# Performance work log

Measured on AMD Instinct MI355X. Metric: run time of the kernel, lower is better.

Reference implementation:

```python
import jax, jax.numpy as jnp
import numpy as np

H = 256       # hidden_dim
DICT = 30     # dict_size
SOS = 1       # symb2int['<sos>']

def gru_cell(x, h, Wih, Whh, bih, bhh):
    # PyTorch GRU cell math
    gi = x @ Wih.T + bih
    gh = h @ Whh.T + bhh
    ir, iz, inn = jnp.split(gi, 3, axis=-1)
    hr, hz, hn = jnp.split(gh, 3, axis=-1)
    r = jax.nn.sigmoid(ir + hr)
    z = jax.nn.sigmoid(iz + hz)
    n = jnp.tanh(inn + r * hn)
    return (1.0 - z) * n + z * h

def run_gru(xs, h0, Wih, Whh, bih, bhh):
    # xs: [T, B, F] -> outputs [T, B, Hc], final hidden [B, Hc]
    def step(h, x):
        h = gru_cell(x, h, Wih, Whh, bih, bhh)
        return h, h
    hT, out = jax.lax.scan(step, h0, xs)
    return out, hT

def setup_inputs() -> dict:
    key = jax.random.key(0)
    ks = jax.random.split(key, 24)
    B, T, L = 128, 512, 64
    se = 1.0 / np.sqrt(H)        # encoder GRU init scale
    sd = 1.0 / np.sqrt(2 * H)    # decoder GRU / linears scale
    def r(k, shape, sc):
        return jax.random.normal(k, shape, jnp.float32) * sc
    return {
        "x": jax.random.normal(ks[0], (B, T, 2), jnp.float32),
        "target_seq": jax.random.randint(ks[1], (B, L), 0, DICT),
        # encoder GRU, forward direction
        "enc_Wih_f": r(ks[2], (3 * H, 2), se), "enc_Whh_f": r(ks[3], (3 * H, H), se),
        "enc_bih_f": r(ks[4], (3 * H,), se),   "enc_bhh_f": r(ks[5], (3 * H,), se),
        # encoder GRU, backward direction
        "enc_Wih_b": r(ks[6], (3 * H, 2), se), "enc_Whh_b": r(ks[7], (3 * H, H), se),
        "enc_bih_b": r(ks[8], (3 * H,), se),   "enc_bhh_b": r(ks[9], (3 * H,), se),
        # decoder embedding + GRU (hidden 2H)
        "emb": r(ks[10], (DICT, H), 1.0),
        "dec_Wih": r(ks[11], (6 * H, H), sd),     "dec_Whh": r(ks[12], (6 * H, 2 * H), sd),
        "dec_bih": r(ks[13], (6 * H,), sd),       "dec_bhh": r(ks[14], (6 * H,), sd),
        # hidden2query, att_combine, fc
        "Wq": r(ks[15], (2 * H, 2 * H), sd), "bq": r(ks[16], (2 * H,), sd),
        "Wc": r(ks[17], (H, 4 * H), sd),     "bc": r(ks[18], (H,), sd),
        "Wf": r(ks[19], (DICT, H), se),      "bf": r(ks[20], (DICT,), se),
    }

def reference(x, target_seq,
              enc_Wih_f, enc_Whh_f, enc_bih_f, enc_bhh_f,
              enc_Wih_b, enc_Whh_b, enc_bih_b, enc_bhh_b,
              emb, dec_Wih, dec_Whh, dec_bih, dec_bhh,
              Wq, bq, Wc, bc, Wf, bf):
    B = x.shape[0]
    xs = jnp.transpose(x, (1, 0, 2))                # [T, B, 2]
    h0 = jnp.zeros((B, H), x.dtype)
    out_f, hf = run_gru(xs, h0, enc_Wih_f, enc_Whh_f, enc_bih_f, enc_bhh_f)
    out_b, hb = run_gru(xs[::-1], h0, enc_Wih_b, enc_Whh_b, enc_bih_b, enc_bhh_b)
    enc_out = jnp.concatenate([out_f, out_b[::-1]], axis=-1)  # [T, B, 2H]
    enc_out = jnp.transpose(enc_out, (1, 0, 2))               # [B, T, 2H]
    hidden = jnp.concatenate([hf, hb], axis=-1)               # [B, 2H]

    # teacher-forced decoder inputs: <sos>, target[0], ..., target[L-2]
    sos = jnp.full((B, 1), SOS, target_seq.dtype)
    toks = jnp.concatenate([sos, target_seq[:, :-1]], axis=1).T  # [L, B]

    def dec_step(h, tok):
        e = emb[tok]                                           # [B, H]
        h = gru_cell(e, h, dec_Wih, dec_Whh, dec_bih, dec_bhh) # [B, 2H]
        q = h @ Wq.T + bq                                      # hidden2query
        w = jax.nn.softmax(jnp.einsum('bh,bth->bt', q, enc_out), axis=-1)
        ctx = jnp.einsum('bt,bth->bh', w, enc_out)             # [B, 2H]
        o = jnp.concatenate([h, ctx], axis=-1) @ Wc.T + bc     # att_combine
        logits = o @ Wf.T + bf                                 # fc
        return h, (logits, w)

    hT, (logits, ws) = jax.lax.scan(dec_step, hidden, toks)
    vec_out = jnp.transpose(logits, (1, 0, 2))   # [B, L, DICT]
    attn = jnp.transpose(ws, (1, 2, 0))          # [B, T, L]
    return vec_out, hT[None], attn
```

## Files before the change

kernel.cpp:

```cpp
#include <hip/hip_runtime.h>
#include <hip/hip_bf16.h>

typedef unsigned int u32;
typedef unsigned short u16;
typedef _Float16 f16;
typedef f16 f16x2 __attribute__((ext_vector_type(2)));

#define BB 128
#define TT 512
#define HE 256
#define G3E 768
#define HD 512
#define G3D 1536
#define LL 64
#define NDICT 30
#define EMBD 256

__device__ __forceinline__ float fexp2(float v){
#if __has_builtin(__builtin_amdgcn_exp2f)
  return __builtin_amdgcn_exp2f(v);
#else
  return exp2f(v);
#endif
}
__device__ __forceinline__ float frcp(float v){
#if __has_builtin(__builtin_amdgcn_rcpf)
  return __builtin_amdgcn_rcpf(v);
#else
  return 1.f/v;
#endif
}
__device__ __forceinline__ float sigm(float v){
  return frcp(1.f + fexp2(-1.4426950408889634f*v));
}
__device__ __forceinline__ float ftanh(float v){
  float e = fexp2(fminf(v, 40.f)*2.8853901631790583f);
  return (e - 1.f)*frcp(e + 1.f);
}
__device__ __forceinline__ u16 f2bf(float f){
  u32 u = __float_as_uint(f);
  u = (u + 0x7FFFu + ((u >> 16) & 1u)) >> 16;
  return (u16)u;
}
__device__ __forceinline__ float bf2f(u16 h){ return __uint_as_float(((u32)h) << 16); }
__device__ __forceinline__ u32 pkh2(float a, float b){
  u16 lo = __builtin_bit_cast(u16, (f16)a);
  u16 hi = __builtin_bit_cast(u16, (f16)b);
  return (u32)lo | ((u32)hi << 16);
}
__device__ __forceinline__ f16x2 bc2(u32 v){ return __builtin_bit_cast(f16x2, v); }

__device__ __forceinline__ void unp8(uint4 v, float* d){
  d[0]=__uint_as_float((v.x&0xffffu)<<16); d[1]=__uint_as_float(v.x&0xffff0000u);
  d[2]=__uint_as_float((v.y&0xffffu)<<16); d[3]=__uint_as_float(v.y&0xffff0000u);
  d[4]=__uint_as_float((v.z&0xffffu)<<16); d[5]=__uint_as_float(v.z&0xffff0000u);
  d[6]=__uint_as_float((v.w&0xffffu)<<16); d[7]=__uint_as_float(v.w&0xffff0000u);
}

__device__ __forceinline__ ushort4 pk4(float a, float b, float c, float d){
  ushort4 r; r.x=f2bf(a); r.y=f2bf(b); r.z=f2bf(c); r.w=f2bf(d); return r;
}

__device__ __forceinline__ float dot2f(u32 w, f16x2 h, float acc){
#if __has_builtin(__builtin_amdgcn_fdot2)
  return __builtin_amdgcn_fdot2(__builtin_bit_cast(f16x2, w), h, acc, false);
#else
  f16x2 wv = __builtin_bit_cast(f16x2, w);
  acc = fmaf((float)wv.x, (float)h.x, acc);
  return fmaf((float)wv.y, (float)h.y, acc);
#endif
}
__device__ __forceinline__ void dot_u4(uint4 wv, uint4 hv, float& acc){
  acc = dot2f(wv.x, bc2(hv.x), acc);
  acc = dot2f(wv.y, bc2(hv.y), acc);
  acc = dot2f(wv.z, bc2(hv.z), acc);
  acc = dot2f(wv.w, bc2(hv.w), acc);
}

#define INNER16(Q0,Q1)                                              \
  _Pragma("unroll 8")                                               \
  for (int k = 0; k < 32; ++k){                                     \
    float4 a4 = *(const float4*)&A_s[k*68 + (Q0)*4];                \
    float4 b4 = *(const float4*)&B_s[k*68 + (Q1)*4];                \
    acc[0] =fmaf(a4.x,b4.x,acc[0]);  acc[1] =fmaf(a4.x,b4.y,acc[1]); \
    acc[2] =fmaf(a4.x,b4.z,acc[2]);  acc[3] =fmaf(a4.x,b4.w,acc[3]); \
    acc[4] =fmaf(a4.y,b4.x,acc[4]);  acc[5] =fmaf(a4.y,b4.y,acc[5]); \
    acc[6] =fmaf(a4.y,b4.z,acc[6]);  acc[7] =fmaf(a4.y,b4.w,acc[7]); \
    acc[8] =fmaf(a4.z,b4.x,acc[8]);  acc[9] =fmaf(a4.z,b4.y,acc[9]); \
    acc[10]=fmaf(a4.z,b4.z,acc[10]); acc[11]=fmaf(a4.z,b4.w,acc[11]);\
    acc[12]=fmaf(a4.w,b4.x,acc[12]); acc[13]=fmaf(a4.w,b4.y,acc[13]);\
    acc[14]=fmaf(a4.w,b4.z,acc[14]); acc[15]=fmaf(a4.w,b4.w,acc[15]);\
  }

__global__ __launch_bounds__(256) void k_transpose(const float* __restrict__ src,
                                                   float* __restrict__ dst, int R, int C){
  int idx = blockIdx.x*256 + threadIdx.x;
  if (idx < R*C){
    int r = idx / C, c = idx - r*C;
    dst[(size_t)c*R + r] = src[idx];
  }
}

__global__ __launch_bounds__(256) void k_prep_wenc(const float* __restrict__ WF,
                                                   const float* __restrict__ WB,
                                                   uint4* __restrict__ dst){
  int idx = blockIdx.x*256 + threadIdx.x;
  int dir = idx / 24576, rem = idx - dir*24576;
  int i = rem / 768, j = rem - i*768;
  const float* s = (dir ? WB : WF) + (size_t)j*HE + i*8;
  uint4 v; v.x=pkh2(s[0],s[1]); v.y=pkh2(s[2],s[3]); v.z=pkh2(s[4],s[5]); v.w=pkh2(s[6],s[7]);
  dst[idx] = v;
}

__global__ __launch_bounds__(256) void k_prep_wdec(const float* __restrict__ src,
                                                   uint4* __restrict__ dst){
  int idx = blockIdx.x*256 + threadIdx.x;
  int lane = idx & 63;
  int ci = lane & 7, kq = lane >> 3;
  int rest = idx >> 6;
  int u = rest & 7, g = (rest >> 3) % 3, cg = rest / 24;
  int row = g*512 + cg*8 + ci;
  int col = kq*64 + u*8;
  const float* s = src + (size_t)row*HD + col;
  uint4 v; v.x=pkh2(s[0],s[1]); v.y=pkh2(s[2],s[3]); v.z=pkh2(s[4],s[5]); v.w=pkh2(s[6],s[7]);
  dst[idx] = v;
}

__global__ __launch_bounds__(256) void k_gi_tab(const float* __restrict__ emb,
                                                const float* __restrict__ Wih,
                                                const float* __restrict__ bih,
                                                float* __restrict__ gi){
  int v = blockIdx.x, gy = blockIdx.y;
  int g = gy*256 + threadIdx.x;
  __shared__ float e_s[EMBD];
  if (threadIdx.x < EMBD) e_s[threadIdx.x] = emb[(size_t)v*EMBD + threadIdx.x];
  __syncthreads();
  const float4* w4 = (const float4*)(Wih + (size_t)g*EMBD);
  float acc = 0.f;
  #pragma unroll 8
  for (int k = 0; k < EMBD/4; ++k){
    float4 w = w4[k];
    float4 h = *(const float4*)&e_s[k*4];
    acc = fmaf(w.x,h.x,fmaf(w.y,h.y,fmaf(w.z,h.z,fmaf(w.w,h.w,acc))));
  }
  gi[(size_t)v*G3D + g] = acc + bih[g];
}

__global__ __launch_bounds__(256) void k_h0cvt(const float* __restrict__ src,
                                               f16* __restrict__ dst){
  int i = blockIdx.x*256 + threadIdx.x;
  dst[i] = (f16)src[i];
}

__global__ __launch_bounds__(768, 3) void k_enc_p(
    const float* __restrict__ x,
    const uint4* __restrict__ Wp,
    const float* __restrict__ WihF, const float* __restrict__ WihB,
    const float* __restrict__ bihF, const float* __restrict__ bhhF,
    const float* __restrict__ bihB, const float* __restrict__ bhhB,
    u16* __restrict__ enc_out, float* __restrict__ h0out)
{
  const int b   = blockIdx.x >> 1;
  const int dir = blockIdx.x & 1;
  const int j   = threadIdx.x;
  const float* Wih = dir ? WihB : WihF;
  const float* bih = dir ? bihB : bihF;
  const float* bhh = dir ? bhhB : bhhF;

  __shared__ __align__(16) f16 h_lds[HE];
  __shared__ float gh[G3E];
  __shared__ float wv0[G3E], wv1[G3E], bis[G3E], bhs[G3E];

  uint4 w[32];
  {
    const uint4* wsrc = Wp + (size_t)dir*24576 + j;
    #pragma unroll
    for (int i = 0; i < 32; ++i) w[i] = wsrc[(size_t)i*768];
  }
  wv0[j] = Wih[j*2+0]; wv1[j] = Wih[j*2+1];
  bis[j] = bih[j];     bhs[j] = bhh[j];
  if (j < HE) h_lds[j] = (f16)0.f;
  float h_own = 0.f;
  __syncthreads();

  for (int t = 0; t < TT; ++t){
    const int tt = dir ? (TT-1-t) : t;
    const float x0 = x[((size_t)b*TT + tt)*2 + 0];
    const float x1 = x[((size_t)b*TT + tt)*2 + 1];

    float a0=0.f, a1=0.f, a2=0.f, a3=0.f;
    const uint4* hv = (const uint4*)h_lds;
    #pragma unroll
    for (int i = 0; i < 32; ++i){
      uint4 h4 = hv[i];
      uint4 wi = w[i];
      a0 = dot2f(wi.x, bc2(h4.x), a0);
      a1 = dot2f(wi.y, bc2(h4.y), a1);
      a2 = dot2f(wi.z, bc2(h4.z), a2);
      a3 = dot2f(wi.w, bc2(h4.w), a3);
    }
    gh[j] = (a0+a1)+(a2+a3);
    __syncthreads();
    if (j < HE){
      float gr = wv0[j]*x0 + wv1[j]*x1 + bis[j] + gh[j] + bhs[j];
      float gz = wv0[j+HE]*x0 + wv1[j+HE]*x1 + bis[j+HE] + gh[j+HE] + bhs[j+HE];
      float r = sigm(gr), z = sigm(gz);
      float gin = wv0[j+2*HE]*x0 + wv1[j+2*HE]*x1 + bis[j+2*HE];
      float n = ftanh(gin + r*(gh[j+2*HE] + bhs[j+2*HE]));
      float hnew = (1.f - z)*n + z*h_own;
      h_own = hnew;
      h_lds[j] = (f16)hnew;
      enc_out[((size_t)b*TT + tt)*HD + dir*HE + j] = f2bf(hnew);
    }
    __syncthreads();
  }
  if (j < HE) h0out[(size_t)b*HD + dir*HE + j] = h_own;
}

__global__ __launch_bounds__(256, 2) void k_dstep(
    const int* __restrict__ tgt, const float* __restrict__ gi_tab,
    const uint4* __restrict__ Wd2, const float* __restrict__ bhh,
    const f16* __restrict__ h_prev, f16* __restrict__ h_next,
    float* __restrict__ Hall, int l)
{
  const int bg = blockIdx.x & 3, cg = blockIdx.x >> 2;
  const int tid = threadIdx.x;
  const int ci = tid & 7, kq = (tid >> 3) & 7, bq = tid >> 6;

  __shared__ __align__(16) f16 h_s[32][HD];
  __shared__ float p_s[3][32][8][8];
  __shared__ int tok_s[32];

  uint4 w[24];
  {
    const uint4* wp = Wd2 + (size_t)cg*24*64 + (kq*8 + ci);
    #pragma unroll
    for (int i = 0; i < 24; ++i) w[i] = wp[(size_t)i*64];
  }
  {
    const uint4* hsrc = (const uint4*)(h_prev + (size_t)bg*32*HD);
    uint4* hdst = (uint4*)&h_s[0][0];
    #pragma unroll
    for (int i = 0; i < 8; ++i) hdst[tid + i*256] = hsrc[tid + i*256];
  }
  if (tid < 32) tok_s[tid] = (l == 0) ? 1 : tgt[(size_t)(bg*32 + tid)*LL + l - 1];
  __syncthreads();

  #pragma unroll
  for (int nb = 0; nb < 8; ++nb){
    const int b = bq*8 + nb;
    const uint4* hv = (const uint4*)&h_s[b][kq*64];
    float x0 = 0.f, x1 = 0.f, x2 = 0.f;
    #pragma unroll
    for (int u = 0; u < 8; ++u){
      uint4 hh = hv[u];
      dot_u4(w[u],      hh, x0);
      dot_u4(w[8 + u],  hh, x1);
      dot_u4(w[16 + u], hh, x2);
    }
    p_s[0][b][ci][kq] = x0;
    p_s[1][b][ci][kq] = x1;
    p_s[2][b][ci][kq] = x2;
  }
  __syncthreads();

  {
    const int b = tid >> 3, cl = tid & 7;
    const int C = cg*8 + cl;
    float s0 = 0.f, s1 = 0.f, s2 = 0.f;
    #pragma unroll
    for (int k = 0; k < 8; ++k){
      s0 += p_s[0][b][cl][k];
      s1 += p_s[1][b][cl][k];
      s2 += p_s[2][b][cl][k];
    }
    const int tok = tok_s[b];
    const float* gp = gi_tab + (size_t)tok*G3D + C;
    float r = sigm(gp[0]    + s0 + bhh[C]);
    float z = sigm(gp[HD]   + s1 + bhh[HD + C]);
    float n = ftanh(gp[2*HD] + r*(s2 + bhh[2*HD + C]));
    float hp = (float)h_s[b][C];
    float hnew = (1.f - z)*n + z*hp;
    const int gb = bg*32 + b;
    h_next[(size_t)gb*HD + C] = (f16)hnew;
    Hall[((size_t)l*BB + gb)*HD + C] = hnew;
  }
}

__global__ __launch_bounds__(256) void k_query(const float* __restrict__ Hall,
                                               const float* __restrict__ WqT,
                                               const float* __restrict__ bq,
                                               u16* __restrict__ Qbf){
  const int rt = blockIdx.x, nt = blockIdx.y;
  const int tid = threadIdx.x;
  __shared__ float A_s[32*68];
  __shared__ float B_s[32*68];
  const int rq = tid >> 4, nq = tid & 15;
  const int i = tid >> 2, jj = tid & 3;
  const int i2 = tid >> 3, jj2 = tid & 7;
  float acc[16] = {};
  for (int kc = 0; kc < 16; ++kc){
    __syncthreads();
    {
      const float* src = Hall + (size_t)(rt*64 + i)*HD + kc*32 + jj*8;
      float4 v0 = *(const float4*)src, v1 = *(const float4*)(src+4);
      A_s[(jj*8+0)*68+i]=v0.x; A_s[(jj*8+1)*68+i]=v0.y;
      A_s[(jj*8+2)*68+i]=v0.z; A_s[(jj*8+3)*68+i]=v0.w;
      A_s[(jj*8+4)*68+i]=v1.x; A_s[(jj*8+5)*68+i]=v1.y;
      A_s[(jj*8+6)*68+i]=v1.z; A_s[(jj*8+7)*68+i]=v1.w;
    }
    {
      const float* src = WqT + (size_t)(kc*32 + i2)*HD + nt*64 + jj2*8;
      *(float4*)&B_s[i2*68 + jj2*8]     = *(const float4*)src;
      *(float4*)&B_s[i2*68 + jj2*8 + 4] = *(const float4*)(src+4);
    }
    __syncthreads();
    INNER16(rq, nq)
  }
  const int n0 = nt*64 + nq*4;
  float4 bv = *(const float4*)&bq[n0];
  #pragma unroll
  for (int r = 0; r < 4; ++r){
    u16* dst = Qbf + (size_t)(rt*64 + rq*4 + r)*HD + n0;
    *(ushort4*)dst = pk4(acc[r*4+0]+bv.x, acc[r*4+1]+bv.y,
                         acc[r*4+2]+bv.z, acc[r*4+3]+bv.w);
  }
}

__global__ __launch_bounds__(256) void k_scores(const u16* __restrict__ Qbf,
                                                const u16* __restrict__ enc,
                                                float* __restrict__ Sbuf){
  const int bI = blockIdx.x, tt = blockIdx.y;
  const int tid = threadIdx.x;
  __shared__ float A_s[32*68];
  __shared__ float B_s[32*68];
  const int lq = tid >> 4, tq = tid & 15;
  const int i = tid >> 2, jj = tid & 3;
  float acc[16] = {};
  for (int kc = 0; kc < 16; ++kc){
    __syncthreads();
    float tmp[8];
    {
      uint4 va = *(const uint4*)(Qbf + ((size_t)i*BB + bI)*HD + kc*32 + jj*8);
      unp8(va, tmp);
      #pragma unroll
      for (int m = 0; m < 8; ++m) A_s[(jj*8+m)*68 + i] = tmp[m];
    }
    {
      uint4 vb = *(const uint4*)(enc + ((size_t)bI*TT + tt*64 + i)*HD + kc*32 + jj*8);
      unp8(vb, tmp);
      #pragma unroll
      for (int m = 0; m < 8; ++m) B_s[(jj*8+m)*68 + i] = tmp[m];
    }
    __syncthreads();
    INNER16(lq, tq)
  }
  #pragma unroll
  for (int r = 0; r < 4; ++r){
    float4 o = make_float4(acc[r*4+0],acc[r*4+1],acc[r*4+2],acc[r*4+3]);
    *(float4*)&Sbuf[((size_t)bI*LL + lq*4+r)*TT + tt*64 + tq*4] = o;
  }
}

__global__ __launch_bounds__(64) void k_softmax(const float* __restrict__ Sbuf,
                                                u16* __restrict__ Pbf){
  const int row = blockIdx.x;
  const int lane = threadIdx.x;
  const float* s = Sbuf + (size_t)row*TT;
  float v[8]; float m = -1e30f;
  #pragma unroll
  for (int i = 0; i < 8; ++i){ v[i] = s[lane + i*64]; m = fmaxf(m, v[i]); }
  #pragma unroll
  for (int o = 32; o; o >>= 1) m = fmaxf(m, __shfl_xor(m, o));
  float Z = 0.f;
  #pragma unroll
  for (int i = 0; i < 8; ++i){ v[i] = fexp2(1.4426950408889634f*(v[i] - m)); Z += v[i]; }
  #pragma unroll
  for (int o = 32; o; o >>= 1) Z += __shfl_xor(Z, o);
  float inv = frcp(Z);
  u16* p = Pbf + (size_t)row*TT;
  #pragma unroll
  for (int i = 0; i < 8; ++i) p[lane + i*64] = f2bf(v[i]*inv);
}

__global__ __launch_bounds__(256) void k_attn_tr(const u16* __restrict__ Pbf,
                                                 float* __restrict__ att){
  const int bI = blockIdx.x, tt = blockIdx.y;
  const int tid = threadIdx.x;
  __shared__ u16 tile[64][72];
  {
    const int i = tid >> 2, jj = tid & 3;
    #pragma unroll
    for (int rep = 0; rep < 2; ++rep){
      int ch = jj + rep*4;
      uint4 v = *(const uint4*)(Pbf + ((size_t)bI*LL + i)*TT + tt*64 + ch*8);
      *(uint4*)&tile[i][ch*8] = v;
    }
  }
  __syncthreads();
  const int t = tid >> 2, jl = tid & 3;
  #pragma unroll
  for (int rep = 0; rep < 4; ++rep){
    int l0 = jl*16 + rep*4;
    float4 o;
    o.x = bf2f(tile[l0+0][t]); o.y = bf2f(tile[l0+1][t]);
    o.z = bf2f(tile[l0+2][t]); o.w = bf2f(tile[l0+3][t]);
    *(float4*)&att[((size_t)bI*TT + tt*64 + t)*LL + l0] = o;
  }
}

__global__ __launch_bounds__(256) void k_ctx(const u16* __restrict__ Pbf,
                                             const u16* __restrict__ enc,
                                             u16* __restrict__ ctxb){
  const int bI = blockIdx.x, nt = blockIdx.y;
  const int tid = threadIdx.x;
  __shared__ float A_s[32*68];
  __shared__ float B_s[32*68];
  const int lq = tid >> 4, nq = tid & 15;
  const int i = tid >> 2, jj = tid & 3;
  const int i2 = tid >> 3, jj2 = tid & 7;
  float acc[16] = {};
  for (int tc = 0; tc < 16; ++tc){
    __syncthreads();
    {
      float tmp[8];
      uint4 va = *(const uint4*)(Pbf + ((size_t)bI*LL + i)*TT + tc*32 + jj*8);
      unp8(va, tmp);
      #pragma unroll
      for (int m = 0; m < 8; ++m) A_s[(jj*8+m)*68 + i] = tmp[m];
    }
    {
      float tmp[8];
      uint4 vb = *(const uint4*)(enc + ((size_t)bI*TT + tc*32 + i2)*HD + nt*64 + jj2*8);
      unp8(vb, tmp);
      *(float4*)&B_s[i2*68 + jj2*8]     = make_float4(tmp[0],tmp[1],tmp[2],tmp[3]);
      *(float4*)&B_s[i2*68 + jj2*8 + 4] = make_float4(tmp[4],tmp[5],tmp[6],tmp[7]);
    }
    __syncthreads();
    INNER16(lq, nq)
  }
  const int n0 = nt*64 + nq*4;
  #pragma unroll
  for (int r = 0; r < 4; ++r){
    int ll = lq*4 + r;
    u16* dst = ctxb + ((size_t)ll*BB + bI)*HD + n0;
    *(ushort4*)dst = pk4(acc[r*4+0], acc[r*4+1], acc[r*4+2], acc[r*4+3]);
  }
}

__global__ __launch_bounds__(256) void k_outc(const float* __restrict__ Hall,
                                              const u16* __restrict__ ctxb,
                                              const float* __restrict__ WcT,
                                              const float* __restrict__ bc,
                                              float* __restrict__ obuf){
  const int rt = blockIdx.x, nt = blockIdx.y;
  const int tid = threadIdx.x;
  __shared__ float A_s[32*68];
  __shared__ float B_s[32*68];
  const int rq = tid >> 4, nq = tid & 15;
  const int i = tid >> 2, jj = tid & 3;
  const int i2 = tid >> 3, jj2 = tid & 7;
  float acc[16] = {};
  for (int kc = 0; kc < 32; ++kc){
    __syncthreads();
    if (kc < 16){
      const float* src = Hall + (size_t)(rt*64 + i)*HD + kc*32 + jj*8;
      float4 v0 = *(const float4*)src, v1 = *(const float4*)(src+4);
      A_s[(jj*8+0)*68+i]=v0.x; A_s[(jj*8+1)*68+i]=v0.y;
      A_s[(jj*8+2)*68+i]=v0.z; A_s[(jj*8+3)*68+i]=v0.w;
      A_s[(jj*8+4)*68+i]=v1.x; A_s[(jj*8+5)*68+i]=v1.y;
      A_s[(jj*8+6)*68+i]=v1.z; A_s[(jj*8+7)*68+i]=v1.w;
    } else {
      float tmp[8];
      uint4 v = *(const uint4*)(ctxb + (size_t)(rt*64 + i)*HD + (kc-16)*32 + jj*8);
      unp8(v, tmp);
      #pragma unroll
      for (int m = 0; m < 8; ++m) A_s[(jj*8+m)*68 + i] = tmp[m];
    }
    {
      const float* src = WcT + (size_t)(kc*32 + i2)*256 + nt*64 + jj2*8;
      *(float4*)&B_s[i2*68 + jj2*8]     = *(const float4*)src;
      *(float4*)&B_s[i2*68 + jj2*8 + 4] = *(const float4*)(src+4);
    }
    __syncthreads();
    INNER16(rq, nq)
  }
  const int n0 = nt*64 + nq*4;
  float4 bv = *(const float4*)&bc[n0];
  #pragma unroll
  for (int r = 0; r < 4; ++r){
    float4 o = make_float4(acc[r*4+0]+bv.x, acc[r*4+1]+bv.y,
                           acc[r*4+2]+bv.z, acc[r*4+3]+bv.w);
    *(float4*)&obuf[(size_t)(rt*64 + rq*4 + r)*256 + n0] = o;
  }
}

__global__ __launch_bounds__(256) void k_fc(const float* __restrict__ obuf,
                                            const float* __restrict__ Wf,
                                            const float* __restrict__ bfv,
                                            float* __restrict__ out_vec){
  const int rt = blockIdx.x;
  const int tid = threadIdx.x;
  __shared__ float w_s[30*260];
  for (int rr = 0; rr < 30; ++rr) w_s[rr*260 + tid] = Wf[(size_t)rr*256 + tid];
  __syncthreads();
  const int rl = tid >> 2, dq = tid & 3;
  const int r = rt*64 + rl;
  float acc[8] = {};
  for (int k = 0; k < 256; k += 4){
    float4 o4 = *(const float4*)&obuf[(size_t)r*256 + k];
    #pragma unroll
    for (int jq = 0; jq < 8; ++jq){
      int d = dq*8 + jq;
      if (d < 30){
        float4 w4 = *(const float4*)&w_s[d*260 + k];
        acc[jq] = fmaf(o4.x,w4.x,fmaf(o4.y,w4.y,fmaf(o4.z,w4.z,fmaf(o4.w,w4.w,acc[jq]))));
      }
    }
  }
  const int b = r & 127, l = r >> 7;
  #pragma unroll
  for (int jq = 0; jq < 8; ++jq){
    int d = dq*8 + jq;
    if (d < 30) out_vec[((size_t)b*LL + l)*NDICT + d] = acc[jq] + bfv[d];
  }
}

__global__ __launch_bounds__(256) void k_copy(const float* __restrict__ src,
                                              float* __restrict__ dst, int n){
  int i = blockIdx.x*256 + threadIdx.x;
  if (i < n) dst[i] = src[i];
}

extern "C" void kernel_launch(void* const* d_in, const int* in_sizes, int n_in,
                              void* d_out, int out_size, void* d_ws, size_t ws_size,
                              hipStream_t stream)
{
  const float* x     = (const float*)d_in[0];
  const int*   tgt   = (const int*)  d_in[1];
  const float* eWihF = (const float*)d_in[2];
  const float* eWhhF = (const float*)d_in[3];
  const float* ebihF = (const float*)d_in[4];
  const float* ebhhF = (const float*)d_in[5];
  const float* eWihB = (const float*)d_in[6];
  const float* eWhhB = (const float*)d_in[7];
  const float* ebihB = (const float*)d_in[8];
  const float* ebhhB = (const float*)d_in[9];
  const float* emb   = (const float*)d_in[10];
  const float* dWih  = (const float*)d_in[11];
  const float* dWhh  = (const float*)d_in[12];
  const float* dbih  = (const float*)d_in[13];
  const float* dbhh  = (const float*)d_in[14];
  const float* Wq    = (const float*)d_in[15];
  const float* bq    = (const float*)d_in[16];
  const float* Wc    = (const float*)d_in[17];
  const float* bc    = (const float*)d_in[18];
  const float* Wf    = (const float*)d_in[19];
  const float* bfv   = (const float*)d_in[20];

  char* w = (char*)d_ws;
  uint4* Wpenc = (uint4*)w; w += 786432;
  uint4* Wpdec = (uint4*)w; w += 1572864;
  float* WqT   = (float*)w; w += 1048576;
  float* WcT   = (float*)w; w += 1048576;
  float* gi_t  = (float*)w; w += 184320;
  float* h0buf = (float*)w; w += 262144;
  f16*   h16A  = (f16*)w; w += 131072;
  f16*   h16B  = (f16*)w; w += 131072;
  float* Hall  = (float*)w; w += 16777216;
  u16*   Qbf   = (u16*)w;
  u16*   Pbf   = (u16*)w; w += 8388608;
  float* Sbuf  = (float*)w;
  u16*   ctxb  = (u16*)w; w += 8388608;
  float* obuf  = (float*)w; w += 8388608;
  u16*   encb  = (u16*)w; w += 67108864;

  float* out     = (float*)d_out;
  float* out_vec = out;
  float* out_hT  = out + (size_t)BB*LL*NDICT;
  float* out_att = out_hT + (size_t)BB*HD;

  k_prep_wenc<<<192, 256, 0, stream>>>(eWhhF, eWhhB, Wpenc);
  k_prep_wdec<<<384, 256, 0, stream>>>(dWhh, Wpdec);
  k_transpose<<<(HD*HD+255)/256, 256, 0, stream>>>(Wq, WqT, HD, HD);
  k_transpose<<<(256*1024+255)/256, 256, 0, stream>>>(Wc, WcT, 256, 1024);
  k_gi_tab<<<dim3(NDICT, 6), 256, 0, stream>>>(emb, dWih, dbih, gi_t);

  k_enc_p<<<BB*2, G3E, 0, stream>>>(x, Wpenc, eWihF, eWihB,
                                    ebihF, ebhhF, ebihB, ebhhB, encb, h0buf);

  k_h0cvt<<<256, 256, 0, stream>>>(h0buf, h16A);
  for (int l = 0; l < LL; ++l){
    const f16* hp = (l & 1) ? h16B : h16A;
    f16*       hn = (l & 1) ? h16A : h16B;
    k_dstep<<<256, 256, 0, stream>>>(tgt, gi_t, Wpdec, dbhh, hp, hn, Hall, l);
  }

  k_query<<<dim3(128,8), 256, 0, stream>>>(Hall, WqT, bq, Qbf);
  k_scores<<<dim3(128,8), 256, 0, stream>>>(Qbf, encb, Sbuf);
  k_softmax<<<BB*LL, 64, 0, stream>>>(Sbuf, Pbf);
  k_attn_tr<<<dim3(128,8), 256, 0, stream>>>(Pbf, out_att);
  k_ctx<<<dim3(128,8), 256, 0, stream>>>(Pbf, encb, ctxb);
  k_outc<<<dim3(128,4), 256, 0, stream>>>(Hall, ctxb, WcT, bc, obuf);
  k_fc<<<BB, 256, 0, stream>>>(obuf, Wf, bfv, out_vec);
  k_copy<<<(BB*HD+255)/256, 256, 0, stream>>>(Hall + (size_t)63*BB*HD, out_hT, BB*HD);
}
```

Measured before the change: 1.327 ms.

## Switch attention GEMMs to packed fp16 dot2 and streamline encoder gate math

```diff
diff --git a/kernel.cpp b/kernel.cpp
--- a/kernel.cpp
+++ b/kernel.cpp
@@ -37,28 +37,27 @@
   float e = fexp2(fminf(v, 40.f)*2.8853901631790583f);
   return (e - 1.f)*frcp(e + 1.f);
 }
-__device__ __forceinline__ u16 f2bf(float f){
-  u32 u = __float_as_uint(f);
-  u = (u + 0x7FFFu + ((u >> 16) & 1u)) >> 16;
-  return (u16)u;
-}
-__device__ __forceinline__ float bf2f(u16 h){ return __uint_as_float(((u32)h) << 16); }
+__device__ __forceinline__ u16 f2h(float f){ return __builtin_bit_cast(u16, (f16)f); }
+__device__ __forceinline__ float h2f(u16 b){ return (float)__builtin_bit_cast(f16, b); }
 __device__ __forceinline__ u32 pkh2(float a, float b){
   u16 lo = __builtin_bit_cast(u16, (f16)a);
   u16 hi = __builtin_bit_cast(u16, (f16)b);
   return (u32)lo | ((u32)hi << 16);
 }
+__device__ __forceinline__ u32 pkrtz(float a, float b){
+  return __builtin_bit_cast(u32, __builtin_amdgcn_cvt_pkrtz(a, b));
+}
 __device__ __forceinline__ f16x2 bc2(u32 v){ return __builtin_bit_cast(f16x2, v); }
 
-__device__ __forceinline__ void unp8(uint4 v, float* d){
-  d[0]=__uint_as_float((v.x&0xffffu)<<16); d[1]=__uint_as_float(v.x&0xffff0000u);
-  d[2]=__uint_as_float((v.y&0xffffu)<<16); d[3]=__uint_as_float(v.y&0xffff0000u);
-  d[4]=__uint_as_float((v.z&0xffffu)<<16); d[5]=__uint_as_float(v.z&0xffff0000u);
-  d[6]=__uint_as_float((v.w&0xffffu)<<16); d[7]=__uint_as_float(v.w&0xffff0000u);
-}
-
-__device__ __forceinline__ ushort4 pk4(float a, float b, float c, float d){
-  ushort4 r; r.x=f2bf(a); r.y=f2bf(b); r.z=f2bf(c); r.w=f2bf(d); return r;
+__device__ __forceinline__ void unp8h(uint4 v, float* d){
+  f16x2 p;
+  p = bc2(v.x); d[0]=(float)p.x; d[1]=(float)p.y;
+  p = bc2(v.y); d[2]=(float)p.x; d[3]=(float)p.y;
+  p = bc2(v.z); d[4]=(float)p.x; d[5]=(float)p.y;
+  p = bc2(v.w); d[6]=(float)p.x; d[7]=(float)p.y;
+}
+__device__ __forceinline__ ushort4 hpk4(float a, float b, float c, float d){
+  ushort4 r; r.x=f2h(a); r.y=f2h(b); r.z=f2h(c); r.w=f2h(d); return r;
 }
 
 __device__ __forceinline__ float dot2f(u32 w, f16x2 h, float acc){
@@ -69,6 +68,9 @@
   acc = fmaf((float)wv.x, (float)h.x, acc);
   return fmaf((float)wv.y, (float)h.y, acc);
 #endif
+}
+__device__ __forceinline__ float dot2h(u32 a, u32 b, float acc){
+  return dot2f(a, bc2(b), acc);
 }
 __device__ __forceinline__ void dot_u4(uint4 wv, uint4 hv, float& acc){
   acc = dot2f(wv.x, bc2(hv.x), acc);
@@ -92,12 +94,28 @@
     acc[14]=fmaf(a4.w,b4.z,acc[14]); acc[15]=fmaf(a4.w,b4.w,acc[15]);\
   }
 
-__global__ __launch_bounds__(256) void k_transpose(const float* __restrict__ src,
-                                                   float* __restrict__ dst, int R, int C){
+#define INNER8P(Q0,Q1)                                                  \
+  _Pragma("unroll")                                                     \
+  for (int kp = 0; kp < 16; ++kp){                                      \
+    uint4 a2 = *(const uint4*)&A2_s[kp*68 + (Q0)*4];                    \
+    uint4 b2 = *(const uint4*)&B2_s[kp*68 + (Q1)*4];                    \
+    acc[0] =dot2h(a2.x,b2.x,acc[0]);  acc[1] =dot2h(a2.x,b2.y,acc[1]);  \
+    acc[2] =dot2h(a2.x,b2.z,acc[2]);  acc[3] =dot2h(a2.x,b2.w,acc[3]);  \
+    acc[4] =dot2h(a2.y,b2.x,acc[4]);  acc[5] =dot2h(a2.y,b2.y,acc[5]);  \
+    acc[6] =dot2h(a2.y,b2.z,acc[6]);  acc[7] =dot2h(a2.y,b2.w,acc[7]);  \
+    acc[8] =dot2h(a2.z,b2.x,acc[8]);  acc[9] =dot2h(a2.z,b2.y,acc[9]);  \
+    acc[10]=dot2h(a2.z,b2.z,acc[10]); acc[11]=dot2h(a2.z,b2.w,acc[11]); \
+    acc[12]=dot2h(a2.w,b2.x,acc[12]); acc[13]=dot2h(a2.w,b2.y,acc[13]); \
+    acc[14]=dot2h(a2.w,b2.z,acc[14]); acc[15]=dot2h(a2.w,b2.w,acc[15]); \
+  }
+
+__global__ __launch_bounds__(256) void k_prep_pairT(const float* __restrict__ src,
+                                                    u32* __restrict__ dst, int N, int K){
   int idx = blockIdx.x*256 + threadIdx.x;
-  if (idx < R*C){
-    int r = idx / C, c = idx - r*C;
-    dst[(size_t)c*R + r] = src[idx];
+  int KP = K >> 1;
+  if (idx < N*KP){
+    int n = idx / KP, kp = idx - n*KP;
+    dst[(size_t)kp*N + n] = pkh2(src[(size_t)n*K + 2*kp], src[(size_t)n*K + 2*kp + 1]);
   }
 }
 
@@ -168,8 +186,8 @@
   const float* bhh = dir ? bhhB : bhhF;
 
   __shared__ __align__(16) f16 h_lds[HE];
-  __shared__ float gh[G3E];
-  __shared__ float wv0[G3E], wv1[G3E], bis[G3E], bhs[G3E];
+  __shared__ float gh[2*HE];
+  __shared__ float gin_s[HE], ghn_s[HE];
 
   uint4 w[32];
   {
@@ -177,8 +195,9 @@
     #pragma unroll
     for (int i = 0; i < 32; ++i) w[i] = wsrc[(size_t)i*768];
   }
-  wv0[j] = Wih[j*2+0]; wv1[j] = Wih[j*2+1];
-  bis[j] = bih[j];     bhs[j] = bhh[j];
+  const float wv0r = Wih[j*2+0], wv1r = Wih[j*2+1];
+  const float bi = bih[j], bh = bhh[j];
+  const float badd = bi + bh;
   if (j < HE) h_lds[j] = (f16)0.f;
   float h_own = 0.f;
   __syncthreads();
@@ -199,18 +218,23 @@
       a2 = dot2f(wi.z, bc2(h4.z), a2);
       a3 = dot2f(wi.w, bc2(h4.w), a3);
     }
-    gh[j] = (a0+a1)+(a2+a3);
+    const float acc = (a0+a1)+(a2+a3);
+    const float xp = fmaf(wv0r, x0, wv1r*x1);
+    if (j < 2*HE){
+      gh[j] = acc + xp + badd;
+    } else {
+      ghn_s[j-2*HE] = acc + bh;
+      gin_s[j-2*HE] = xp + bi;
+    }
     __syncthreads();
     if (j < HE){
-      float gr = wv0[j]*x0 + wv1[j]*x1 + bis[j] + gh[j] + bhs[j];
-      float gz = wv0[j+HE]*x0 + wv1[j+HE]*x1 + bis[j+HE] + gh[j+HE] + bhs[j+HE];
-      float r = sigm(gr), z = sigm(gz);
-      float gin = wv0[j+2*HE]*x0 + wv1[j+2*HE]*x1 + bis[j+2*HE];
-      float n = ftanh(gin + r*(gh[j+2*HE] + bhs[j+2*HE]));
+      float r = sigm(gh[j]);
+      float z = sigm(gh[j+HE]);
+      float n = ftanh(gin_s[j] + r*ghn_s[j]);
       float hnew = (1.f - z)*n + z*h_own;
       h_own = hnew;
       h_lds[j] = (f16)hnew;
-      enc_out[((size_t)b*TT + tt)*HD + dir*HE + j] = f2bf(hnew);
+      enc_out[((size_t)b*TT + tt)*HD + dir*HE + j] = f2h(hnew);
     }
     __syncthreads();
   }
@@ -288,72 +312,72 @@
 }
 
 __global__ __launch_bounds__(256) void k_query(const float* __restrict__ Hall,
-                                               const float* __restrict__ WqT,
+                                               const u32* __restrict__ Wq2,
                                                const float* __restrict__ bq,
-                                               u16* __restrict__ Qbf){
+                                               u16* __restrict__ Qh){
   const int rt = blockIdx.x, nt = blockIdx.y;
   const int tid = threadIdx.x;
-  __shared__ float A_s[32*68];
-  __shared__ float B_s[32*68];
+  __shared__ u32 A2_s[16*68];
+  __shared__ u32 B2_s[16*68];
   const int rq = tid >> 4, nq = tid & 15;
   const int i = tid >> 2, jj = tid & 3;
-  const int i2 = tid >> 3, jj2 = tid & 7;
+  const int i3 = tid >> 4, n4 = tid & 15;
   float acc[16] = {};
   for (int kc = 0; kc < 16; ++kc){
     __syncthreads();
     {
       const float* src = Hall + (size_t)(rt*64 + i)*HD + kc*32 + jj*8;
       float4 v0 = *(const float4*)src, v1 = *(const float4*)(src+4);
-      A_s[(jj*8+0)*68+i]=v0.x; A_s[(jj*8+1)*68+i]=v0.y;
-      A_s[(jj*8+2)*68+i]=v0.z; A_s[(jj*8+3)*68+i]=v0.w;
-      A_s[(jj*8+4)*68+i]=v1.x; A_s[(jj*8+5)*68+i]=v1.y;
-      A_s[(jj*8+6)*68+i]=v1.z; A_s[(jj*8+7)*68+i]=v1.w;
+      A2_s[(jj*4+0)*68+i] = pkrtz(v0.x, v0.y);
+      A2_s[(jj*4+1)*68+i] = pkrtz(v0.z, v0.w);
+      A2_s[(jj*4+2)*68+i] = pkrtz(v1.x, v1.y);
+      A2_s[(jj*4+3)*68+i] = pkrtz(v1.z, v1.w);
     }
     {
-      const float* src = WqT + (size_t)(kc*32 + i2)*HD + nt*64 + jj2*8;
-      *(float4*)&B_s[i2*68 + jj2*8]     = *(const float4*)src;
-      *(float4*)&B_s[i2*68 + jj2*8 + 4] = *(const float4*)(src+4);
-    }
-    __syncthreads();
-    INNER16(rq, nq)
+      uint4 v = *(const uint4*)(Wq2 + (size_t)(kc*16 + i3)*HD + nt*64 + n4*4);
+      *(uint4*)&B2_s[i3*68 + n4*4] = v;
+    }
+    __syncthreads();
+    INNER8P(rq, nq)
   }
   const int n0 = nt*64 + nq*4;
   float4 bv = *(const float4*)&bq[n0];
   #pragma unroll
   for (int r = 0; r < 4; ++r){
-    u16* dst = Qbf + (size_t)(rt*64 + rq*4 + r)*HD + n0;
-    *(ushort4*)dst = pk4(acc[r*4+0]+bv.x, acc[r*4+1]+bv.y,
-                         acc[r*4+2]+bv.z, acc[r*4+3]+bv.w);
-  }
-}
-
-__global__ __launch_bounds__(256) void k_scores(const u16* __restrict__ Qbf,
+    u16* dst = Qh + (size_t)(rt*64 + rq*4 + r)*HD + n0;
+    *(ushort4*)dst = hpk4(acc[r*4+0]+bv.x, acc[r*4+1]+bv.y,
+                          acc[r*4+2]+bv.z, acc[r*4+3]+bv.w);
+  }
+}
+
+__global__ __launch_bounds__(256) void k_scores(const u16* __restrict__ Qh,
                                                 const u16* __restrict__ enc,
                                                 float* __restrict__ Sbuf){
   const int bI = blockIdx.x, tt = blockIdx.y;
   const int tid = threadIdx.x;
-  __shared__ float A_s[32*68];
-  __shared__ float B_s[32*68];
+  __shared__ u32 A2_s[16*68];
+  __shared__ u32 B2_s[16*68];
   const int lq = tid >> 4, tq = tid & 15;
   const int i = tid >> 2, jj = tid & 3;
   float acc[16] = {};
   for (int kc = 0; kc < 16; ++kc){
     __syncthreads();
-    float tmp[8];
     {
-      uint4 va = *(const uint4*)(Qbf + ((size_t)i*BB + bI)*HD + kc*32 + jj*8);
-      unp8(va, tmp);
-      #pragma unroll
-      for (int m = 0; m < 8; ++m) A_s[(jj*8+m)*68 + i] = tmp[m];
+      uint4 va = *(const uint4*)(Qh + ((size_t)i*BB + bI)*HD + kc*32 + jj*8);
+      A2_s[(jj*4+0)*68+i] = va.x;
+      A2_s[(jj*4+1)*68+i] = va.y;
+      A2_s[(jj*4+2)*68+i] = va.z;
+      A2_s[(jj*4+3)*68+i] = va.w;
     }
     {
       uint4 vb = *(const uint4*)(enc + ((size_t)bI*TT + tt*64 + i)*HD + kc*32 + jj*8);
-      unp8(vb, tmp);
-      #pragma unroll
-      for (int m = 0; m < 8; ++m) B_s[(jj*8+m)*68 + i] = tmp[m];
-    }
-    __syncthreads();
-    INNER16(lq, tq)
+      B2_s[(jj*4+0)*68+i] = vb.x;
+      B2_s[(jj*4+1)*68+i] = vb.y;
+      B2_s[(jj*4+2)*68+i] = vb.z;
+      B2_s[(jj*4+3)*68+i] = vb.w;
+    }
+    __syncthreads();
+    INNER8P(lq, tq)
   }
   #pragma unroll
   for (int r = 0; r < 4; ++r){
@@ -363,7 +387,7 @@
 }
 
 __global__ __launch_bounds__(64) void k_softmax(const float* __restrict__ Sbuf,
-                                                u16* __restrict__ Pbf){
+                                                u16* __restrict__ Ph){
   const int row = blockIdx.x;
   const int lane = threadIdx.x;
   const float* s = Sbuf + (size_t)row*TT;
@@ -378,12 +402,12 @@
   #pragma unroll
   for (int o = 32; o; o >>= 1) Z += __shfl_xor(Z, o);
   float inv = frcp(Z);
-  u16* p = Pbf + (size_t)row*TT;
-  #pragma unroll
-  for (int i = 0; i < 8; ++i) p[lane + i*64] = f2bf(v[i]*inv);
-}
-
-__global__ __launch_bounds__(256) void k_attn_tr(const u16* __restrict__ Pbf,
+  u16* p = Ph + (size_t)row*TT;
+  #pragma unroll
+  for (int i = 0; i < 8; ++i) p[lane + i*64] = f2h(v[i]*inv);
+}
+
+__global__ __launch_bounds__(256) void k_attn_tr(const u16* __restrict__ Ph,
                                                  float* __restrict__ att){
   const int bI = blockIdx.x, tt = blockIdx.y;
   const int tid = threadIdx.x;
@@ -393,7 +417,7 @@
     #pragma unroll
     for (int rep = 0; rep < 2; ++rep){
       int ch = jj + rep*4;
-      uint4 v = *(const uint4*)(Pbf + ((size_t)bI*LL + i)*TT + tt*64 + ch*8);
+      uint4 v = *(const uint4*)(Ph + ((size_t)bI*LL + i)*TT + tt*64 + ch*8);
       *(uint4*)&tile[i][ch*8] = v;
     }
   }
@@ -403,15 +427,15 @@
   for (int rep = 0; rep < 4; ++rep){
     int l0 = jl*16 + rep*4;
     float4 o;
-    o.x = bf2f(tile[l0+0][t]); o.y = bf2f(tile[l0+1][t]);
-    o.z = bf2f(tile[l0+2][t]); o.w = bf2f(tile[l0+3][t]);
+    o.x = h2f(tile[l0+0][t]); o.y = h2f(tile[l0+1][t]);
+    o.z = h2f(tile[l0+2][t]); o.w = h2f(tile[l0+3][t]);
     *(float4*)&att[((size_t)bI*TT + tt*64 + t)*LL + l0] = o;
   }
 }
 
-__global__ __launch_bounds__(256) void k_ctx(const u16* __restrict__ Pbf,
+__global__ __launch_bounds__(256) void k_ctx(const u16* __restrict__ Ph,
                                              const u16* __restrict__ enc,
-                                             u16* __restrict__ ctxb){
+                                             u16* __restrict__ ctxh){
   const int bI = blockIdx.x, nt = blockIdx.y;
   const int tid = threadIdx.x;
   __shared__ float A_s[32*68];
@@ -424,15 +448,15 @@
     __syncthreads();
     {
       float tmp[8];
-      uint4 va = *(const uint4*)(Pbf + ((size_t)bI*LL + i)*TT + tc*32 + jj*8);
-      unp8(va, tmp);
+      uint4 va = *(const uint4*)(Ph + ((size_t)bI*LL + i)*TT + tc*32 + jj*8);
+      unp8h(va, tmp);
       #pragma unroll
       for (int m = 0; m < 8; ++m) A_s[(jj*8+m)*68 + i] = tmp[m];
     }
     {
       float tmp[8];
       uint4 vb = *(const uint4*)(enc + ((size_t)bI*TT + tc*32 + i2)*HD + nt*64 + jj2*8);
-      unp8(vb, tmp);
+      unp8h(vb, tmp);
       *(float4*)&B_s[i2*68 + jj2*8]     = make_float4(tmp[0],tmp[1],tmp[2],tmp[3]);
       *(float4*)&B_s[i2*68 + jj2*8 + 4] = make_float4(tmp[4],tmp[5],tmp[6],tmp[7]);
     }
@@ -443,47 +467,46 @@
   #pragma unroll
   for (int r = 0; r < 4; ++r){
     int ll = lq*4 + r;
-    u16* dst = ctxb + ((size_t)ll*BB + bI)*HD + n0;
-    *(ushort4*)dst = pk4(acc[r*4+0], acc[r*4+1], acc[r*4+2], acc[r*4+3]);
+    u16* dst = ctxh + ((size_t)ll*BB + bI)*HD + n0;
+    *(ushort4*)dst = hpk4(acc[r*4+0], acc[r*4+1], acc[r*4+2], acc[r*4+3]);
   }
 }
 
 __global__ __launch_bounds__(256) void k_outc(const float* __restrict__ Hall,
-                                              const u16* __restrict__ ctxb,
-                                              const float* __restrict__ WcT,
+                                              const u16* __restrict__ ctxh,
+                                              const u32* __restrict__ Wc2,
                                               const float* __restrict__ bc,
                                               float* __restrict__ obuf){
   const int rt = blockIdx.x, nt = blockIdx.y;
   const int tid = threadIdx.x;
-  __shared__ float A_s[32*68];
-  __shared__ float B_s[32*68];
+  __shared__ u32 A2_s[16*68];
+  __shared__ u32 B2_s[16*68];
   const int rq = tid >> 4, nq = tid & 15;
   const int i = tid >> 2, jj = tid & 3;
-  const int i2 = tid >> 3, jj2 = tid & 7;
+  const int i3 = tid >> 4, n4 = tid & 15;
   float acc[16] = {};
   for (int kc = 0; kc < 32; ++kc){
     __syncthreads();
     if (kc < 16){
       const float* src = Hall + (size_t)(rt*64 + i)*HD + kc*32 + jj*8;
       float4 v0 = *(const float4*)src, v1 = *(const float4*)(src+4);
-      A_s[(jj*8+0)*68+i]=v0.x; A_s[(jj*8+1)*68+i]=v0.y;
-      A_s[(jj*8+2)*68+i]=v0.z; A_s[(jj*8+3)*68+i]=v0.w;
-      A_s[(jj*8+4)*68+i]=v1.x; A_s[(jj*8+5)*68+i]=v1.y;
-      A_s[(jj*8+6)*68+i]=v1.z; A_s[(jj*8+7)*68+i]=v1.w;
+      A2_s[(jj*4+0)*68+i] = pkrtz(v0.x, v0.y);
+      A2_s[(jj*4+1)*68+i] = pkrtz(v0.z, v0.w);
+      A2_s[(jj*4+2)*68+i] = pkrtz(v1.x, v1.y);
+      A2_s[(jj*4+3)*68+i] = pkrtz(v1.z, v1.w);
     } else {
-      float tmp[8];
-      uint4 v = *(const uint4*)(ctxb + (size_t)(rt*64 + i)*HD + (kc-16)*32 + jj*8);
-      unp8(v, tmp);
-      #pragma unroll
-      for (int m = 0; m < 8; ++m) A_s[(jj*8+m)*68 + i] = tmp[m];
+      uint4 v = *(const uint4*)(ctxh + (size_t)(rt*64 + i)*HD + (kc-16)*32 + jj*8);
+      A2_s[(jj*4+0)*68+i] = v.x;
+      A2_s[(jj*4+1)*68+i] = v.y;
+      A2_s[(jj*4+2)*68+i] = v.z;
+      A2_s[(jj*4+3)*68+i] = v.w;
     }
     {
-      const float* src = WcT + (size_t)(kc*32 + i2)*256 + nt*64 + jj2*8;
-      *(float4*)&B_s[i2*68 + jj2*8]     = *(const float4*)src;
-      *(float4*)&B_s[i2*68 + jj2*8 + 4] = *(const float4*)(src+4);
-    }
-    __syncthreads();
-    INNER16(rq, nq)
+      uint4 v = *(const uint4*)(Wc2 + (size_t)(kc*16 + i3)*256 + nt*64 + n4*4);
+      *(uint4*)&B2_s[i3*68 + n4*4] = v;
+    }
+    __syncthreads();
+    INNER8P(rq, nq)
   }
   const int n0 = nt*64 + nq*4;
   float4 bv = *(const float4*)&bc[n0];
@@ -561,19 +584,19 @@
   char* w = (char*)d_ws;
   uint4* Wpenc = (uint4*)w; w += 786432;
   uint4* Wpdec = (uint4*)w; w += 1572864;
-  float* WqT   = (float*)w; w += 1048576;
-  float* WcT   = (float*)w; w += 1048576;
+  u32*   Wq2   = (u32*)w;  w += 524288;
+  u32*   Wc2   = (u32*)w;  w += 524288;
   float* gi_t  = (float*)w; w += 184320;
   float* h0buf = (float*)w; w += 262144;
   f16*   h16A  = (f16*)w; w += 131072;
   f16*   h16B  = (f16*)w; w += 131072;
   float* Hall  = (float*)w; w += 16777216;
-  u16*   Qbf   = (u16*)w;
-  u16*   Pbf   = (u16*)w; w += 8388608;
+  u16*   Qh    = (u16*)w;
+  u16*   Ph    = (u16*)w; w += 8388608;
   float* Sbuf  = (float*)w;
-  u16*   ctxb  = (u16*)w; w += 8388608;
+  u16*   ctxh  = (u16*)w; w += 8388608;
   float* obuf  = (float*)w; w += 8388608;
-  u16*   encb  = (u16*)w; w += 67108864;
+  u16*   ench  = (u16*)w; w += 67108864;
 
   float* out     = (float*)d_out;
   float* out_vec = out;
@@ -582,12 +605,12 @@
 
   k_prep_wenc<<<192, 256, 0, stream>>>(eWhhF, eWhhB, Wpenc);
   k_prep_wdec<<<384, 256, 0, stream>>>(dWhh, Wpdec);
-  k_transpose<<<(HD*HD+255)/256, 256, 0, stream>>>(Wq, WqT, HD, HD);
-  k_transpose<<<(256*1024+255)/256, 256, 0, stream>>>(Wc, WcT, 256, 1024);
+  k_prep_pairT<<<512, 256, 0, stream>>>(Wq, Wq2, HD, HD);
+  k_prep_pairT<<<512, 256, 0, stream>>>(Wc, Wc2, 256, 1024);
   k_gi_tab<<<dim3(NDICT, 6), 256, 0, stream>>>(emb, dWih, dbih, gi_t);
 
   k_enc_p<<<BB*2, G3E, 0, stream>>>(x, Wpenc, eWihF, eWihB,
-                                    ebihF, ebhhF, ebihB, ebhhB, encb, h0buf);
+                                    ebihF, ebhhF, ebihB, ebhhB, ench, h0buf);
 
   k_h0cvt<<<256, 256, 0, stream>>>(h0buf, h16A);
   for (int l = 0; l < LL; ++l){
@@ -596,12 +619,12 @@
     k_dstep<<<256, 256, 0, stream>>>(tgt, gi_t, Wpdec, dbhh, hp, hn, Hall, l);
   }
 
-  k_query<<<dim3(128,8), 256, 0, stream>>>(Hall, WqT, bq, Qbf);
-  k_scores<<<dim3(128,8), 256, 0, stream>>>(Qbf, encb, Sbuf);
-  k_softmax<<<BB*LL, 64, 0, stream>>>(Sbuf, Pbf);
-  k_attn_tr<<<dim3(128,8), 256, 0, stream>>>(Pbf, out_att);
-  k_ctx<<<dim3(128,8), 256, 0, stream>>>(Pbf, encb, ctxb);
-  k_outc<<<dim3(128,4), 256, 0, stream>>>(Hall, ctxb, WcT, bc, obuf);
+  k_query<<<dim3(128,8), 256, 0, stream>>>(Hall, Wq2, bq, Qh);
+  k_scores<<<dim3(128,8), 256, 0, stream>>>(Qh, ench, Sbuf);
+  k_softmax<<<BB*LL, 64, 0, stream>>>(Sbuf, Ph);
+  k_attn_tr<<<dim3(128,8), 256, 0, stream>>>(Ph, out_att);
+  k_ctx<<<dim3(128,8), 256, 0, stream>>>(Ph, ench, ctxh);
+  k_outc<<<dim3(128,4), 256, 0, stream>>>(Hall, ctxh, Wc2, bc, obuf);
   k_fc<<<BB, 256, 0, stream>>>(obuf, Wf, bfv, out_vec);
   k_copy<<<(BB*HD+255)/256, 256, 0, stream>>>(Hall + (size_t)63*BB*HD, out_hT, BB*HD);
 }
```

Result: faster. 1.222 ms (-7.9%).
